# Optimization experiments

Measured on AMD Instinct MI355X. Metric: run time of the kernel, lower is better.

The kernel has to match this reference:

```python
import jax, jax.numpy as jnp
import numpy as np

IOU_LOW = 0.5   # <= low  -> background (-1)
IOU_HIGH = 0.6  # (low, high) -> neutral (-1e8)
NEUTRAL = -1e8


def setup_inputs() -> dict:
    key = jax.random.key(0)
    k1, k2, k3, k4, k5 = jax.random.split(key, 5)
    B, N, M = 16, 32768, 64
    # Proposals: XYXY boxes inside an ~800x800 image (built from rand fills).
    p_xy1 = jax.random.uniform(k1, (B, N, 2), dtype=jnp.float32) * 600.0
    p_wh = jax.random.uniform(k2, (B, N, 2), dtype=jnp.float32) * 200.0 + 1.0
    proposals = jnp.concatenate([p_xy1, p_xy1 + p_wh], axis=-1)  # (B, N, 4)
    # GT boxes: XYXY + float class id in last column (all valid here; the
    # reference still implements the class==-1 padding mask like the torch code).
    g_xy1 = jax.random.uniform(k3, (B, M, 2), dtype=jnp.float32) * 600.0
    g_wh = jax.random.uniform(k4, (B, M, 2), dtype=jnp.float32) * 200.0 + 1.0
    g_cls = jax.random.randint(k5, (B, M, 1), 0, 20).astype(jnp.float32)
    gt_boxes = jnp.concatenate([g_xy1, g_xy1 + g_wh, g_cls], axis=-1)  # (B, M, 5)
    return {"proposals": proposals, "gt_boxes": gt_boxes}


def _pairwise_iou(b1, b2):
    # b1: (N, 4), b2: (M, 4), XYXY -> (N, M)
    area1 = (b1[:, 2] - b1[:, 0]) * (b1[:, 3] - b1[:, 1])  # (N,)
    area2 = (b2[:, 2] - b2[:, 0]) * (b2[:, 3] - b2[:, 1])  # (M,)
    x1 = jnp.maximum(b1[:, None, 0], b2[None, :, 0])
    y1 = jnp.maximum(b1[:, None, 1], b2[None, :, 1])
    x2 = jnp.minimum(b1[:, None, 2], b2[None, :, 2])
    y2 = jnp.minimum(b1[:, None, 3], b2[None, :, 3])
    inter = jnp.maximum(x2 - x1, 0.0) * jnp.maximum(y2 - y1, 0.0)
    return inter / (area1[:, None] + area2[None, :] - inter)


def _match_one(props, gtb):
    # props: (N, 4), gtb: (M, 5) with class==-1 marking padded GT boxes.
    valid = gtb[:, 4] != -1.0  # (M,)
    iou = _pairwise_iou(props, gtb[:, :4])  # (N, M)
    iou = jnp.where(valid[None, :], iou, -1.0)
    match_quality = jnp.max(iou, axis=1)  # (N,)
    matched_idxs = jnp.argmax(iou, axis=1)  # (N,)
    matched = gtb[matched_idxs]  # (N, 5) gather of boxes+class
    matched = jnp.where((match_quality <= IOU_LOW)[:, None], -1.0, matched)
    neutral = (match_quality > IOU_LOW) & (match_quality < IOU_HIGH)
    matched = jnp.where(neutral[:, None], NEUTRAL, matched)
    # No valid GT at all -> all background (fake boxes/class = -1).
    matched = jnp.where(jnp.any(valid), matched, -1.0)
    return matched


def reference(proposals, gt_boxes):
    # proposals: (B, N, 4), gt_boxes: (B, M, 5) -> matched GT (B, N, 5)
    return jax.vmap(_match_one)(proposals, gt_boxes)
```

## Files before the change

### kernel.cpp

```cpp
#include <hip/hip_runtime.h>

#define BATCH 16
#define NPROP 32768
#define NGT   64
#define BLOCK 256
#define P     2

__global__ __launch_bounds__(BLOCK) void match_kernel(
    const float* __restrict__ props,
    const float* __restrict__ gt,
    float* __restrict__ out)
{
    __shared__ float4 sbox[NGT];
    __shared__ float  sa2[NGT];
    __shared__ float  scls[NGT];

    const int blocksPerBatch = NPROP / (BLOCK * P);
    const int b    = blockIdx.x / blocksPerBatch;
    const int base = (blockIdx.x % blocksPerBatch) * (BLOCK * P);

    if (threadIdx.x < NGT) {
        const float* g = gt + ((size_t)b * NGT + threadIdx.x) * 5;
        float x1 = g[0], y1 = g[1], x2 = g[2], y2 = g[3], c = g[4];
        float a2 = (x2 - x1) * (y2 - y1);
        if (c == -1.0f) { x1 = y1 = x2 = y2 = -1.0e4f; a2 = 1.0f; }
        sbox[threadIdx.x] = make_float4(x1, y1, x2, y2);
        sa2[threadIdx.x]  = a2;
        scls[threadIdx.x] = c;
    }
    __syncthreads();

    const float4* pv = reinterpret_cast<const float4*>(props)
                     + (size_t)b * NPROP + base + threadIdx.x;
    float4 p[P];
    float  a1[P];
    #pragma unroll
    for (int k = 0; k < P; ++k) {
        p[k]  = pv[k * BLOCK];
        a1[k] = (p[k].z - p[k].x) * (p[k].w - p[k].y);
    }

    float bn[P], bd[P];
    int   bi[P];
    #pragma unroll
    for (int k = 0; k < P; ++k) { bn[k] = -1.0f; bd[k] = 1.0f; bi[k] = 0; }

    #pragma unroll 8
    for (int m = 0; m < NGT; ++m) {
        const float4 g  = sbox[m];
        const float  a2 = sa2[m];
        #pragma unroll
        for (int k = 0; k < P; ++k) {
            const float ix1 = fmaxf(p[k].x, g.x);
            const float iy1 = fmaxf(p[k].y, g.y);
            const float ix2 = fminf(p[k].z, g.z);
            const float iy2 = fminf(p[k].w, g.w);
            const float inter = fmaxf(ix2 - ix1, 0.0f) * fmaxf(iy2 - iy1, 0.0f);
            const float den   = (a1[k] + a2) - inter;

            const bool better = inter * bd[k] > bn[k] * den;
            bn[k] = better ? inter : bn[k];
            bd[k] = better ? den   : bd[k];
            bi[k] = better ? m     : bi[k];
        }
    }

    #pragma unroll
    for (int k = 0; k < P; ++k) {
        const float q  = bn[k] / bd[k];
        const float4 g = sbox[bi[k]];
        const float gc = scls[bi[k]];

        const bool bg      = (q <= 0.5f);
        const bool neutral = (q > 0.5f) & (q < 0.6f);
        const float fill   = neutral ? -1.0e8f : -1.0f;
        const bool keep    = !(bg | neutral);

        float* op = out + ((size_t)b * NPROP + base + threadIdx.x + k * BLOCK) * 5;
        op[0] = keep ? g.x : fill;
        op[1] = keep ? g.y : fill;
        op[2] = keep ? g.z : fill;
        op[3] = keep ? g.w : fill;
        op[4] = keep ? gc  : fill;
    }
}

extern "C" void kernel_launch(void* const* d_in, const int* in_sizes, int n_in,
                              void* d_out, int out_size, void* d_ws, size_t ws_size,
                              hipStream_t stream) {
    const float* props = (const float*)d_in[0];
    const float* gt    = (const float*)d_in[1];
    float* out = (float*)d_out;

    const int grid = BATCH * (NPROP / (BLOCK * P));
    match_kernel<<<grid, BLOCK, 0, stream>>>(props, gt, out);
}
```

Measured before the change: 22.68 us.

## Assign adjacent proposals per thread, vectorize output stores, simplify IoU comparison

Each thread now handles two adjacent proposals instead of two proposals a block apart. Their ten output floats are contiguous, so they are written as five float2 stores rather than scalar stride-5 stores. The argmax comparison now tracks the area sum S instead of the union denominator, which saves a subtract per pair. GT areas are read from LDS as float4, and the division happens once at the end as inter/(S-inter). The trade-offs are less coalesced float4 loads of proposals and a comparison that can round slightly differently near ties.

```diff
diff --git a/kernel.cpp b/kernel.cpp
--- a/kernel.cpp
+++ b/kernel.cpp
@@ -12,7 +12,7 @@
     float* __restrict__ out)
 {
     __shared__ float4 sbox[NGT];
-    __shared__ float  sa2[NGT];
+    __shared__ float4 sa2q[NGT / 4];
     __shared__ float  scls[NGT];
 
     const int blocksPerBatch = NPROP / (BLOCK * P);
@@ -25,64 +25,77 @@
         float a2 = (x2 - x1) * (y2 - y1);
         if (c == -1.0f) { x1 = y1 = x2 = y2 = -1.0e4f; a2 = 1.0f; }
         sbox[threadIdx.x] = make_float4(x1, y1, x2, y2);
-        sa2[threadIdx.x]  = a2;
+        reinterpret_cast<float*>(sa2q)[threadIdx.x] = a2;
         scls[threadIdx.x] = c;
     }
     __syncthreads();
 
+    const int n0 = base + 2 * (int)threadIdx.x;
     const float4* pv = reinterpret_cast<const float4*>(props)
-                     + (size_t)b * NPROP + base + threadIdx.x;
+                     + (size_t)b * NPROP + n0;
     float4 p[P];
     float  a1[P];
     #pragma unroll
     for (int k = 0; k < P; ++k) {
-        p[k]  = pv[k * BLOCK];
+        p[k]  = pv[k];
         a1[k] = (p[k].z - p[k].x) * (p[k].w - p[k].y);
     }
 
-    float bn[P], bd[P];
+    float bn[P], bs[P];
     int   bi[P];
     #pragma unroll
-    for (int k = 0; k < P; ++k) { bn[k] = -1.0f; bd[k] = 1.0f; bi[k] = 0; }
+    for (int k = 0; k < P; ++k) { bn[k] = -1.0f; bs[k] = 1.0f; bi[k] = 0; }
 
-    #pragma unroll 8
-    for (int m = 0; m < NGT; ++m) {
-        const float4 g  = sbox[m];
-        const float  a2 = sa2[m];
+    #pragma unroll 4
+    for (int mq = 0; mq < NGT / 4; ++mq) {
+        const float4 a2q = sa2q[mq];
+        const float a2s[4] = { a2q.x, a2q.y, a2q.z, a2q.w };
         #pragma unroll
-        for (int k = 0; k < P; ++k) {
-            const float ix1 = fmaxf(p[k].x, g.x);
-            const float iy1 = fmaxf(p[k].y, g.y);
-            const float ix2 = fminf(p[k].z, g.z);
-            const float iy2 = fminf(p[k].w, g.w);
-            const float inter = fmaxf(ix2 - ix1, 0.0f) * fmaxf(iy2 - iy1, 0.0f);
-            const float den   = (a1[k] + a2) - inter;
+        for (int j = 0; j < 4; ++j) {
+            const int m = mq * 4 + j;
+            const float4 g  = sbox[m];
+            const float  a2 = a2s[j];
+            #pragma unroll
+            for (int k = 0; k < P; ++k) {
+                const float ix1 = fmaxf(p[k].x, g.x);
+                const float iy1 = fmaxf(p[k].y, g.y);
+                const float ix2 = fminf(p[k].z, g.z);
+                const float iy2 = fminf(p[k].w, g.w);
+                const float inter = fmaxf(ix2 - ix1, 0.0f) * fmaxf(iy2 - iy1, 0.0f);
+                const float S     = a1[k] + a2;
 
-            const bool better = inter * bd[k] > bn[k] * den;
-            bn[k] = better ? inter : bn[k];
-            bd[k] = better ? den   : bd[k];
-            bi[k] = better ? m     : bi[k];
+                const bool better = inter * bs[k] > bn[k] * S;
+                bn[k] = better ? inter : bn[k];
+                bs[k] = better ? S     : bs[k];
+                bi[k] = better ? m     : bi[k];
+            }
         }
     }
 
+    float o[P * 5];
     #pragma unroll
     for (int k = 0; k < P; ++k) {
-        const float q  = bn[k] / bd[k];
-        const float4 g = sbox[bi[k]];
-        const float gc = scls[bi[k]];
+        const float den = bs[k] - bn[k];
+        const float q   = bn[k] / den;
+        const float4 g  = sbox[bi[k]];
+        const float  gc = scls[bi[k]];
 
         const bool bg      = (q <= 0.5f);
         const bool neutral = (q > 0.5f) & (q < 0.6f);
         const float fill   = neutral ? -1.0e8f : -1.0f;
         const bool keep    = !(bg | neutral);
 
-        float* op = out + ((size_t)b * NPROP + base + threadIdx.x + k * BLOCK) * 5;
-        op[0] = keep ? g.x : fill;
-        op[1] = keep ? g.y : fill;
-        op[2] = keep ? g.z : fill;
-        op[3] = keep ? g.w : fill;
-        op[4] = keep ? gc  : fill;
+        o[k * 5 + 0] = keep ? g.x : fill;
+        o[k * 5 + 1] = keep ? g.y : fill;
+        o[k * 5 + 2] = keep ? g.z : fill;
+        o[k * 5 + 3] = keep ? g.w : fill;
+        o[k * 5 + 4] = keep ? gc  : fill;
     }
+
+    float2* op2 = reinterpret_cast<float2*>(out + ((size_t)b * NPROP + n0) * 5);
+    #pragma unroll
+    for (int j = 0; j < 5; ++j)
+        op2[j] = make_float2(o[2 * j], o[2 * j + 1]);
 }
 
 extern "C" void kernel_launch(void* const* d_in, const int* in_sizes, int n_in,
```

Measured after the change: 22.89 us. No clear change (+0.9%).
